# Performance work log

Measured on AMD Instinct MI355X. Metric: run time of the kernel, lower is better.

The kernel has to match this reference:

```python
import jax, jax.numpy as jnp
import numpy as np

N = 100000   # nodes
E = 800000   # undirected (unique) edges; directed count = 2*E
DV = 128; DE = 16; DH = 128; DO = 128
G = 64       # graphs in batch


def setup_inputs() -> dict:
    key = jax.random.key(0)
    ks = jax.random.split(key, 8)
    x = jax.random.normal(ks[0], (N, DV), jnp.float32)
    edge_index = jax.random.randint(ks[1], (2, 2 * E), 0, N, dtype=jnp.int32)
    edge_attr = jax.random.normal(ks[2], (E, DE), jnp.float32)
    batch = jnp.sort(jax.random.randint(ks[3], (N,), 0, G, dtype=jnp.int32))
    s = lambda k, shp, fan: jax.random.normal(k, shp, jnp.float32) / np.sqrt(fan)
    W_gcn = s(ks[4], (DV, DH), DV); b_gcn = jnp.zeros((DH,), jnp.float32)
    W_le = s(ks[5], (DE, DH), DE); b_le = jnp.zeros((DH,), jnp.float32)
    W_lin = s(ks[6], (2 * DH, DH), 2 * DH); b_lin = jnp.zeros((DH,), jnp.float32)
    W_out = s(ks[7], (DH, DO), DH); b_out = jnp.zeros((DO,), jnp.float32)
    return dict(x=x, edge_index=edge_index, edge_attr=edge_attr, batch=batch,
                W_gcn=W_gcn, b_gcn=b_gcn, W_le=W_le, b_le=b_le,
                W_lin=W_lin, b_lin=b_lin, W_out=W_out, b_out=b_out)


def reference(x, edge_index, edge_attr, batch,
              W_gcn, b_gcn, W_le, b_le, W_lin, b_lin, W_out, b_out):
    n = x.shape[0]
    loop = jnp.arange(n, dtype=edge_index.dtype)
    src = jnp.concatenate([edge_index[0], loop])  # [2E+N] with self loops
    dst = jnp.concatenate([edge_index[1], loop])

    # ---- GCNConv: symmetric norm, self-loops, lin then aggregate, + bias ----
    xw = x @ W_gcn                                      # [N, DH]
    ones_e = jnp.ones(src.shape[0], jnp.float32)
    deg = jax.ops.segment_sum(ones_e, dst, num_segments=n)  # >=1 via self loops
    dinv = jax.lax.rsqrt(deg)
    norm = dinv[src] * dinv[dst]                        # [2E+N]
    h = jax.ops.segment_sum(norm[:, None] * xw[src], dst, num_segments=n) + b_gcn
    h = jax.nn.relu(h)

    # ---- EdgeGCN: duplicate edge_attr per direction, self-loop attr = ones ----
    ea2 = jnp.repeat(edge_attr, 2, axis=0)              # [2E, DE] interleaved
    ea_full = jnp.concatenate([ea2, jnp.ones((n, edge_attr.shape[1]), jnp.float32)])
    edge_feat = ea_full @ W_le + b_le                   # [2E+N, DH]
    x_j = h[src]                                        # gather source node feats
    msg = jnp.concatenate([x_j, edge_feat], axis=-1) @ W_lin + b_lin
    h2 = jax.ops.segment_sum(msg, dst, num_segments=n)  # aggr='add'
    h2 = jax.nn.relu(h2)

    # ---- global mean pool + final linear ----
    cnt = jax.ops.segment_sum(jnp.ones(n, jnp.float32), batch, num_segments=G)
    pooled = jax.ops.segment_sum(h2, batch, num_segments=G) / jnp.maximum(cnt, 1.0)[:, None]
    return pooled @ W_out + b_out                       # [G, DO]
```

## Files before the change

### kernel.cpp

```cpp
#include <hip/hip_runtime.h>
#include <hip/hip_bf16.h>
#include <cstddef>

typedef unsigned int  u32;
typedef unsigned short u16;
typedef __attribute__((ext_vector_type(8))) short short8;
typedef __attribute__((ext_vector_type(4))) float f32x4;
typedef __attribute__((ext_vector_type(2))) float f32x2;

#define DV 128
#define DH 128
#define DE 16
#define DO 128
#define PSUB 32

__device__ inline float bf_lo(u32 u){ return __uint_as_float(u << 16); }
__device__ inline float bf_hi(u32 u){ return __uint_as_float(u & 0xFFFF0000u); }
__device__ inline u32 fpack2(float a, float b){
  u32 ua = __float_as_uint(a), ub = __float_as_uint(b);
  ua += 0x7FFFu + ((ua >> 16) & 1u);
  ub += 0x7FFFu + ((ub >> 16) & 1u);
  return (ua >> 16) | (ub & 0xFFFF0000u);
}
__device__ inline u16 f2bf(float a){
  u32 ua = __float_as_uint(a); ua += 0x7FFFu + ((ua >> 16) & 1u); return (u16)(ua >> 16);
}

__device__ inline void acc_fp8(u32 s, float& a0, float& a1, float& a2, float& a3){
  f32x2 lo = __builtin_amdgcn_cvt_pk_f32_fp8((int)s, false);
  f32x2 hi = __builtin_amdgcn_cvt_pk_f32_fp8((int)s, true);
  a0 += lo.x; a1 += lo.y; a2 += hi.x; a3 += hi.y;
}
__device__ inline u32 pack_fp8(float a0, float a1, float a2, float a3){
  int o = __builtin_amdgcn_cvt_pk_fp8_f32(a0, a1, 0, false);
  o = __builtin_amdgcn_cvt_pk_fp8_f32(a2, a3, o, true);
  return (u32)o;
}

__global__ void k_init(int* cnt, int n){
  int v = blockIdx.x * blockDim.x + threadIdx.x;
  if (v < n) cnt[v] = 0;
}
__global__ void k_count(const int* dst, int* cnt, int* rank, int e2){
  int j = blockIdx.x * blockDim.x + threadIdx.x;
  if (j < e2) rank[j] = atomicAdd(&cnt[dst[j]], 1);
}
__global__ __launch_bounds__(256) void k_scan1(const int* cnt, int* partial, int* bsums, int n){
  __shared__ int lds[256];
  int t = threadIdx.x;
  int base = blockIdx.x * 1024 + t * 4;
  int v0=0,v1=0,v2=0,v3=0;
  if (base + 3 < n){ int4 q = *(const int4*)(cnt + base); v0=q.x; v1=q.y; v2=q.z; v3=q.w; }
  else {
    if (base + 0 < n) v0 = cnt[base];
    if (base + 1 < n) v1 = cnt[base+1];
    if (base + 2 < n) v2 = cnt[base+2];
  }
  v0 = (v0 + 7) & ~7; v1 = (v1 + 7) & ~7; v2 = (v2 + 7) & ~7; v3 = (v3 + 7) & ~7;
  v1 += v0; v2 += v1; v3 += v2;
  lds[t] = v3; __syncthreads();
  for (int off = 1; off < 256; off <<= 1){
    int x = (t >= off) ? lds[t - off] : 0;
    __syncthreads();
    lds[t] += x;
    __syncthreads();
  }
  int add = (t > 0) ? lds[t - 1] : 0;
  if (base + 3 < n){
    int4 q; q.x = v0+add; q.y = v1+add; q.z = v2+add; q.w = v3+add;
    *(int4*)(partial + base) = q;
  } else {
    if (base + 0 < n) partial[base]   = v0 + add;
    if (base + 1 < n) partial[base+1] = v1 + add;
    if (base + 2 < n) partial[base+2] = v2 + add;
  }
  if (t == 255) bsums[blockIdx.x] = lds[255];
}
__global__ void k_scan2(const int* bsums, int* bexc, int nb){
  __shared__ int lds[128];
  int t = threadIdx.x;
  lds[t] = (t < nb) ? bsums[t] : 0;
  __syncthreads();
  for (int off = 1; off < 128; off <<= 1){
    int x = (t >= off) ? lds[t - off] : 0;
    __syncthreads();
    lds[t] += x;
    __syncthreads();
  }
  if (t < nb) bexc[t] = (t > 0) ? lds[t - 1] : 0;
}
__global__ void k_scan3(const int* partial, const int* bexc, int* row_ptr, int n){
  int i = blockIdx.x * blockDim.x + threadIdx.x;
  if (i < n) row_ptr[i + 1] = partial[i] + bexc[i >> 10];
  if (i == 0) row_ptr[0] = 0;
}
__global__ void k_prep(const int* cnt, float* dinv, float* degf, int n){
  int v = blockIdx.x * blockDim.x + threadIdx.x;
  if (v < n){
    float c = (float)(cnt[v] + 1);
    dinv[v] = rsqrtf(c);
    degf[v] = c;
  }
}
__global__ void k_scatter(const int* src, const int* dst, const int* rank,
                          const int* row_ptr, int2* ce, int e2){
  int j = blockIdx.x * blockDim.x + threadIdx.x;
  if (j < e2){
    int d = dst[j];
    int pos = row_ptr[d] + rank[j];
    ce[pos] = make_int2(src[j], j);
  }
}
__global__ void k_pad(const int* row_ptr, const int* cnt, int2* ce,
                      u32* xws_zrow, u32* h_zrow, int n){
  int v = blockIdx.x * blockDim.x + threadIdx.x;
  if (v < n){
    int s = row_ptr[v] + cnt[v], e = row_ptr[v + 1];
    for (int i = s; i < e; ++i) ce[i] = make_int2(n, 0);
  }
  if (blockIdx.x == 0 && threadIdx.x < 32){
    xws_zrow[threadIdx.x] = 0u;
    h_zrow[threadIdx.x] = 0u;
  }
}

__global__ __launch_bounds__(128) void k_wcombo(const float* W_lin, const float* b_lin,
                                                const float* W_le, const float* b_le, float* Wfull){
  int r = blockIdx.x, c = threadIdx.x;
  if (r < DH){
    Wfull[r * DH + c] = W_lin[r * DH + c];
  } else if (r < DH + DE){
    int i = r - DH;
    float acc = 0.f;
    #pragma unroll 8
    for (int k = 0; k < DH; k += 4){
      float4 wl = *(const float4*)(W_le + i * DH + k);
      acc += wl.x * W_lin[(size_t)(DH + k    ) * DH + c];
      acc += wl.y * W_lin[(size_t)(DH + k + 1) * DH + c];
      acc += wl.z * W_lin[(size_t)(DH + k + 2) * DH + c];
      acc += wl.w * W_lin[(size_t)(DH + k + 3) * DH + c];
    }
    Wfull[r * DH + c] = acc;
  } else if (r == 144){
    float acc = b_lin[c];
    #pragma unroll 8
    for (int k = 0; k < DH; k += 4){
      float4 bl = *(const float4*)(b_le + k);
      acc += bl.x * W_lin[(size_t)(DH + k    ) * DH + c];
      acc += bl.y * W_lin[(size_t)(DH + k + 1) * DH + c];
      acc += bl.z * W_lin[(size_t)(DH + k + 2) * DH + c];
      acc += bl.w * W_lin[(size_t)(DH + k + 3) * DH + c];
    }
    Wfull[r * DH + c] = acc;
  } else {
    Wfull[r * DH + c] = 0.f;
  }
}

template<int K, bool RELU, bool ABF16, bool SCALE, bool OFP8>
__global__ __launch_bounds__(256) void k_gemm_mfma(const void* Ap, const float* W, u32* outb,
                                                   const float* scale, int M){
  constexpr int SA = K + 8;
  constexpr int CS = 136;
  __shared__ u16 Wt[128 * SA];
  __shared__ u16 At[64 * SA];
  int tid = threadIdx.x;
  int row0 = blockIdx.x * 64;

  {
    int c = tid & 127, half = tid >> 7;
    for (int g = half; g < K / 8; g += 2){
      int k0 = g * 8;
      float w0 = W[(size_t)(k0+0)*128 + c], w1 = W[(size_t)(k0+1)*128 + c];
      float w2 = W[(size_t)(k0+2)*128 + c], w3 = W[(size_t)(k0+3)*128 + c];
      float w4 = W[(size_t)(k0+4)*128 + c], w5 = W[(size_t)(k0+5)*128 + c];
      float w6 = W[(size_t)(k0+6)*128 + c], w7 = W[(size_t)(k0+7)*128 + c];
      uint4 pk;
      pk.x = fpack2(w0, w1); pk.y = fpack2(w2, w3);
      pk.z = fpack2(w4, w5); pk.w = fpack2(w6, w7);
      *(uint4*)&Wt[c * SA + k0] = pk;
    }
  }
  constexpr int CH = K / 8;
  for (int idx = tid; idx < 64 * CH; idx += 256){
    int r = idx / CH, ch = idx - r * CH;
    int gr = row0 + r; if (gr > M - 1) gr = M - 1;
    uint4 pk;
    if (ABF16){
      pk = *(const uint4*)((const u16*)Ap + (size_t)gr * K + ch * 8);
    } else {
      const float* A = (const float*)Ap + (size_t)gr * K + ch * 8;
      float4 q0 = *(const float4*)A;
      float4 q1 = *(const float4*)(A + 4);
      pk.x = fpack2(q0.x, q0.y); pk.y = fpack2(q0.z, q0.w);
      pk.z = fpack2(q1.x, q1.y); pk.w = fpack2(q1.z, q1.w);
    }
    *(uint4*)&At[r * SA + ch * 8] = pk;
  }
  __syncthreads();

  int l = tid & 63, w = tid >> 6;
  int m = l & 15, quad = l >> 4;
  f32x4 acc[8];
  #pragma unroll
  for (int ct = 0; ct < 8; ++ct) acc[ct] = (f32x4){0.f, 0.f, 0.f, 0.f};
  #pragma unroll
  for (int ks = 0; ks < K; ks += 32){
    short8 av = *(const short8*)&At[(w * 16 + m) * SA + ks + quad * 8];
    #pragma unroll
    for (int ct = 0; ct < 8; ++ct){
      short8 bv = *(const short8*)&Wt[(ct * 16 + m) * SA + ks + quad * 8];
      acc[ct] = __builtin_amdgcn_mfma_f32_16x16x32_bf16(av, bv, acc[ct], 0, 0, 0);
    }
  }
  __syncthreads();

  u16* Ct = At;
  float sc[4];
  if (SCALE){
    #pragma unroll
    for (int r = 0; r < 4; ++r){
      int gr = row0 + w * 16 + quad * 4 + r;
      sc[r] = scale[gr < M ? gr : (M - 1)];
    }
  }
  #pragma unroll
  for (int ct = 0; ct < 8; ++ct){
    #pragma unroll
    for (int r = 0; r < 4; ++r){
      float vv = acc[ct][r];
      if (SCALE) vv *= sc[r];
      if (RELU)  vv = fmaxf(vv, 0.f);
      Ct[(w * 16 + quad * 4 + r) * CS + ct * 16 + m] = f2bf(vv);
    }
  }
  __syncthreads();
  if (OFP8){
    for (int idx = tid; idx < 64 * 16; idx += 256){
      int r = idx >> 4, c8 = idx & 15;
      int gr = row0 + r;
      if (gr < M){
        uint4 qv = *(const uint4*)&Ct[r * CS + c8 * 8];
        uint2 ov;
        ov.x = (u32)__builtin_amdgcn_cvt_pk_fp8_f32(bf_lo(qv.y), bf_hi(qv.y),
               __builtin_amdgcn_cvt_pk_fp8_f32(bf_lo(qv.x), bf_hi(qv.x), 0, false), true);
        ov.y = (u32)__builtin_amdgcn_cvt_pk_fp8_f32(bf_lo(qv.w), bf_hi(qv.w),
               __builtin_amdgcn_cvt_pk_fp8_f32(bf_lo(qv.z), bf_hi(qv.z), 0, false), true);
        *(uint2*)(outb + (size_t)gr * 32 + c8 * 2) = ov;
      }
    }
  } else {
    for (int idx = tid; idx < 64 * 16; idx += 256){
      int r = idx >> 4, ch = idx & 15;
      int gr = row0 + r;
      if (gr < M){
        uint4 q = *(const uint4*)&Ct[r * CS + ch * 8];
        *(uint4*)(outb + (size_t)gr * 64 + ch * 4) = q;
      }
    }
  }
}

__global__ __launch_bounds__(256) void k_phase1(const u32* xws8, const int* row_ptr, const int2* ce,
                                                const float* dinv, const float* b_gcn, u32* h8, int n){
  int lane = threadIdx.x & 63;
  int ln = lane & 31;
  int v = blockIdx.x * 8 + ((threadIdx.x >> 6) << 1) + (lane >> 5);
  if (v >= n) return;
  u32 sp = xws8[(size_t)v * 32 + ln];
  float a0 = 0.f, a1 = 0.f, a2 = 0.f, a3 = 0.f;
  acc_fp8(sp, a0, a1, a2, a3);
  int e0 = row_ptr[v], e1 = row_ptr[v + 1];
  int i = e0;
  u32 q0=0,q1=0,q2=0,q3=0,q4=0,q5=0,q6=0,q7=0;
  if (i < e1){
    const int4* cp = (const int4*)(ce + i);
    int4 A = cp[0], B = cp[1], C = cp[2], D = cp[3];
    q0 = xws8[(size_t)A.x * 32 + ln]; q1 = xws8[(size_t)A.z * 32 + ln];
    q2 = xws8[(size_t)B.x * 32 + ln]; q3 = xws8[(size_t)B.z * 32 + ln];
    q4 = xws8[(size_t)C.x * 32 + ln]; q5 = xws8[(size_t)C.z * 32 + ln];
    q6 = xws8[(size_t)D.x * 32 + ln]; q7 = xws8[(size_t)D.z * 32 + ln];
  }
  for (; i + 8 < e1; i += 8){
    const int4* cp2 = (const int4*)(ce + i + 8);
    int4 A = cp2[0], B = cp2[1], C = cp2[2], D = cp2[3];
    u32 p0 = xws8[(size_t)A.x * 32 + ln], p1 = xws8[(size_t)A.z * 32 + ln];
    u32 p2 = xws8[(size_t)B.x * 32 + ln], p3 = xws8[(size_t)B.z * 32 + ln];
    u32 p4 = xws8[(size_t)C.x * 32 + ln], p5 = xws8[(size_t)C.z * 32 + ln];
    u32 p6 = xws8[(size_t)D.x * 32 + ln], p7 = xws8[(size_t)D.z * 32 + ln];
    acc_fp8(q0, a0, a1, a2, a3); acc_fp8(q1, a0, a1, a2, a3);
    acc_fp8(q2, a0, a1, a2, a3); acc_fp8(q3, a0, a1, a2, a3);
    acc_fp8(q4, a0, a1, a2, a3); acc_fp8(q5, a0, a1, a2, a3);
    acc_fp8(q6, a0, a1, a2, a3); acc_fp8(q7, a0, a1, a2, a3);
    q0=p0; q1=p1; q2=p2; q3=p3; q4=p4; q5=p5; q6=p6; q7=p7;
  }
  if (i < e1){
    acc_fp8(q0, a0, a1, a2, a3); acc_fp8(q1, a0, a1, a2, a3);
    acc_fp8(q2, a0, a1, a2, a3); acc_fp8(q3, a0, a1, a2, a3);
    acc_fp8(q4, a0, a1, a2, a3); acc_fp8(q5, a0, a1, a2, a3);
    acc_fp8(q6, a0, a1, a2, a3); acc_fp8(q7, a0, a1, a2, a3);
  }
  float dv = dinv[v];
  float4 bg = *(const float4*)(b_gcn + ln * 4);
  a0 = fmaxf(fmaf(dv, a0, bg.x), 0.f);
  a1 = fmaxf(fmaf(dv, a1, bg.y), 0.f);
  a2 = fmaxf(fmaf(dv, a2, bg.z), 0.f);
  a3 = fmaxf(fmaf(dv, a3, bg.w), 0.f);
  h8[(size_t)v * 32 + ln] = pack_fp8(a0, a1, a2, a3);
}

__global__ __launch_bounds__(256) void k_phase2(const u32* h8, const int* row_ptr, const int2* ce,
                                                const float* edge_attr, const float* degf,
                                                u16* A2b, int n){
  int lane = threadIdx.x & 63;
  int ln = lane & 31;
  int half = lane >> 5;
  int v = blockIdx.x * 8 + ((threadIdx.x >> 6) << 1) + half;
  if (v >= n) return;
  u32 sp = h8[(size_t)v * 32 + ln];
  float a0 = 0.f, a1 = 0.f, a2 = 0.f, a3 = 0.f;
  acc_fp8(sp, a0, a1, a2, a3);
  float es = 0.f;
  int ch = ln & 15, grp = ln >> 4;
  int e0 = row_ptr[v], e1 = row_ptr[v + 1];
  int i = e0;
  u32 q0=0,q1=0,q2=0,q3=0,q4=0,q5=0,q6=0,q7=0;
  int4 A = {0,0,0,0}, B = {0,0,0,0}, C = {0,0,0,0}, D = {0,0,0,0};
  if (i < e1){
    const int4* cp = (const int4*)(ce + i);
    A = cp[0]; B = cp[1]; C = cp[2]; D = cp[3];
    q0 = h8[(size_t)A.x * 32 + ln]; q1 = h8[(size_t)A.z * 32 + ln];
    q2 = h8[(size_t)B.x * 32 + ln]; q3 = h8[(size_t)B.z * 32 + ln];
    q4 = h8[(size_t)C.x * 32 + ln]; q5 = h8[(size_t)C.z * 32 + ln];
    q6 = h8[(size_t)D.x * 32 + ln]; q7 = h8[(size_t)D.z * 32 + ln];
  }
  for (; i + 8 < e1; i += 8){
    const int4* cp2 = (const int4*)(ce + i + 8);
    int4 A2 = cp2[0], B2 = cp2[1], C2 = cp2[2], D2 = cp2[3];
    int s0x = grp ? C.x : A.x, s0y = grp ? C.y : A.y;
    int s1x = grp ? C.z : A.z, s1y = grp ? C.w : A.w;
    int s2x = grp ? D.x : B.x, s2y = grp ? D.y : B.y;
    int s3x = grp ? D.z : B.z, s3y = grp ? D.w : B.w;
    float v0 = edge_attr[(size_t)(s0y >> 1) * DE + ch];
    float v1 = edge_attr[(size_t)(s1y >> 1) * DE + ch];
    float v2 = edge_attr[(size_t)(s2y >> 1) * DE + ch];
    float v3 = edge_attr[(size_t)(s3y >> 1) * DE + ch];
    u32 p0 = h8[(size_t)A2.x * 32 + ln], p1 = h8[(size_t)A2.z * 32 + ln];
    u32 p2 = h8[(size_t)B2.x * 32 + ln], p3 = h8[(size_t)B2.z * 32 + ln];
    u32 p4 = h8[(size_t)C2.x * 32 + ln], p5 = h8[(size_t)C2.z * 32 + ln];
    u32 p6 = h8[(size_t)D2.x * 32 + ln], p7 = h8[(size_t)D2.z * 32 + ln];
    acc_fp8(q0, a0, a1, a2, a3); acc_fp8(q1, a0, a1, a2, a3);
    acc_fp8(q2, a0, a1, a2, a3); acc_fp8(q3, a0, a1, a2, a3);
    acc_fp8(q4, a0, a1, a2, a3); acc_fp8(q5, a0, a1, a2, a3);
    acc_fp8(q6, a0, a1, a2, a3); acc_fp8(q7, a0, a1, a2, a3);
    es = fmaf((s0x != n) ? 1.f : 0.f, v0, es);
    es = fmaf((s1x != n) ? 1.f : 0.f, v1, es);
    es = fmaf((s2x != n) ? 1.f : 0.f, v2, es);
    es = fmaf((s3x != n) ? 1.f : 0.f, v3, es);
    q0=p0; q1=p1; q2=p2; q3=p3; q4=p4; q5=p5; q6=p6; q7=p7;
    A=A2; B=B2; C=C2; D=D2;
  }
  if (i < e1){
    int s0x = grp ? C.x : A.x, s0y = grp ? C.y : A.y;
    int s1x = grp ? C.z : A.z, s1y = grp ? C.w : A.w;
    int s2x = grp ? D.x : B.x, s2y = grp ? D.y : B.y;
    int s3x = grp ? D.z : B.z, s3y = grp ? D.w : B.w;
    float v0 = edge_attr[(size_t)(s0y >> 1) * DE + ch];
    float v1 = edge_attr[(size_t)(s1y >> 1) * DE + ch];
    float v2 = edge_attr[(size_t)(s2y >> 1) * DE + ch];
    float v3 = edge_attr[(size_t)(s3y >> 1) * DE + ch];
    acc_fp8(q0, a0, a1, a2, a3); acc_fp8(q1, a0, a1, a2, a3);
    acc_fp8(q2, a0, a1, a2, a3); acc_fp8(q3, a0, a1, a2, a3);
    acc_fp8(q4, a0, a1, a2, a3); acc_fp8(q5, a0, a1, a2, a3);
    acc_fp8(q6, a0, a1, a2, a3); acc_fp8(q7, a0, a1, a2, a3);
    es = fmaf((s0x != n) ? 1.f : 0.f, v0, es);
    es = fmaf((s1x != n) ? 1.f : 0.f, v1, es);
    es = fmaf((s2x != n) ? 1.f : 0.f, v2, es);
    es = fmaf((s3x != n) ? 1.f : 0.f, v3, es);
  }
  es += __shfl_xor(es, 16);
  float c0v = __shfl(es, half * 32 + (ln & 7) * 2);
  float c1v = __shfl(es, half * 32 + (ln & 7) * 2 + 1);
  u32* rowp = (u32*)(A2b + (size_t)v * 160);
  uint2 o; o.x = fpack2(a0, a1); o.y = fpack2(a2, a3);
  *(uint2*)(rowp + ln * 2) = o;
  if (ln < 8){
    rowp[64 + ln] = fpack2(c0v + 1.0f, c1v + 1.0f);
  } else if (ln < 16){
    rowp[64 + ln] = (ln == 8) ? (u32)f2bf(degf[v]) : 0u;
  }
}

__global__ void k_starts(const int* batch, int* start, int n, int g){
  int v = blockIdx.x * blockDim.x + threadIdx.x;
  if (v >= n) return;
  int b = batch[v];
  int prev = (v == 0) ? -1 : batch[v - 1];
  for (int q = prev + 1; q <= b; ++q) start[q] = v;
  if (v == n - 1){ for (int q = b + 1; q <= g; ++q) start[q] = n; }
}
__global__ __launch_bounds__(256) void k_pool_a(const u32* h2_b, const int* start, float* partialp){
  __shared__ float2 red[256];
  int g = blockIdx.x >> 5;
  int s = blockIdx.x & (PSUB - 1);
  int s0 = start[g], s1 = start[g + 1];
  int tid = threadIdx.x;
  int cu = tid & 63, rr = tid >> 6;
  float ax = 0.f, ay = 0.f;
  for (int r = s0 + s * 4 + rr; r < s1; r += PSUB * 4){
    u32 q = h2_b[(size_t)r * 64 + cu];
    ax += bf_lo(q); ay += bf_hi(q);
  }
  red[tid] = make_float2(ax, ay);
  __syncthreads();
  if (rr == 0){
    #pragma unroll
    for (int p = 1; p < 4; p++){ float2 o = red[cu + (p << 6)]; ax += o.x; ay += o.y; }
    *(float2*)(partialp + (size_t)blockIdx.x * 128 + cu * 2) = make_float2(ax, ay);
  }
}
__global__ __launch_bounds__(128) void k_poolb_final(const float* partialp, const int* start,
                                                     const float* W_out, const float* b_out,
                                                     float* out){
  __shared__ float pl[DH];
  int g = blockIdx.x, c = threadIdx.x;
  float sum = 0.f;
  #pragma unroll 4
  for (int s = 0; s < PSUB; ++s) sum += partialp[((size_t)g * PSUB + s) * 128 + c];
  int cntg = start[g + 1] - start[g]; if (cntg < 1) cntg = 1;
  pl[c] = sum / (float)cntg;
  __syncthreads();
  float acc = b_out[c];
  for (int k = 0; k < DH; ++k) acc += pl[k] * W_out[k * DO + c];
  out[g * DO + c] = acc;
}

extern "C" void kernel_launch(void* const* d_in, const int* in_sizes, int n_in,
                              void* d_out, int out_size, void* d_ws, size_t ws_size,
                              hipStream_t stream){
  const float* x         = (const float*)d_in[0];
  const int*   edge_index= (const int*)  d_in[1];
  const float* edge_attr = (const float*)d_in[2];
  const int*   batch     = (const int*)  d_in[3];
  const float* W_gcn     = (const float*)d_in[4];
  const float* b_gcn     = (const float*)d_in[5];
  const float* W_le      = (const float*)d_in[6];
  const float* b_le      = (const float*)d_in[7];
  const float* W_lin     = (const float*)d_in[8];
  const float* b_lin     = (const float*)d_in[9];
  const float* W_out     = (const float*)d_in[10];
  const float* b_out     = (const float*)d_in[11];
  float* out = (float*)d_out;

  const int n  = in_sizes[0] / DV;
  const int e2 = in_sizes[1] / 2;
  const int g  = out_size / DO;
  const int* srcp = edge_index;
  const int* dstp = edge_index + e2;
  const int e2pad = e2 + 7 * n + 8;

  char* ws = (char*)d_ws;
  size_t off = 0;
  auto alloc = [&](size_t bytes) -> char* {
    char* p = ws + off; off = (off + bytes + 255) & ~(size_t)255; return p;
  };

  int*   cnt     = (int*)  alloc((size_t)n * 4);
  int*   row_ptr = (int*)  alloc((size_t)(n + 1) * 4);
  int*   rank    = (int*)  alloc((size_t)e2 * 4);
  int*   partial = (int*)  alloc((size_t)n * 4);
  int*   bsums   = (int*)  alloc(512);
  int*   bexc    = (int*)  alloc(512);
  float* dinv    = (float*)alloc((size_t)n * 4);
  float* degf    = (float*)alloc((size_t)n * 4);
  int*   startg  = (int*)  alloc((size_t)(g + 1) * 4);
  float* partialp= (float*)alloc((size_t)g * PSUB * 128 * 4);
  float* Wfull   = (float*)alloc(160 * DH * 4);
  u32*   h8      = (u32*)  alloc((size_t)(n + 1) * 128);
  int2*  ce      = (int2*) alloc((size_t)e2pad * 8);
  u32*   h2_b    = (u32*)  alloc((size_t)n * 64 * 4);
  size_t szXW = (size_t)(n + 1) * 128, szA2 = (size_t)n * 160 * 2;
  char* regionA = alloc(szA2 > szXW ? szA2 : szXW);
  u32* xws8 = (u32*)regionA;
  u16* A2b  = (u16*)regionA;

  const int nb1024 = (n + 1023) / 1024;

  k_init   <<<(n + 255) / 256, 256, 0, stream>>>(cnt, n);
  k_count  <<<(e2 + 255) / 256, 256, 0, stream>>>(dstp, cnt, rank, e2);
  k_scan1  <<<nb1024, 256, 0, stream>>>(cnt, partial, bsums, n);
  k_scan2  <<<1, 128, 0, stream>>>(bsums, bexc, nb1024);
  k_scan3  <<<(n + 255) / 256, 256, 0, stream>>>(partial, bexc, row_ptr, n);
  k_prep   <<<(n + 255) / 256, 256, 0, stream>>>(cnt, dinv, degf, n);
  k_scatter<<<(e2 + 255) / 256, 256, 0, stream>>>(srcp, dstp, rank, row_ptr, ce, e2);
  k_pad    <<<(n + 255) / 256, 256, 0, stream>>>(row_ptr, cnt, ce,
                                                 xws8 + (size_t)n * 32, h8 + (size_t)n * 32, n);
  k_wcombo <<<160, 128, 0, stream>>>(W_lin, b_lin, W_le, b_le, Wfull);

  k_gemm_mfma<DV, false, false, true, true><<<(n + 63) / 64, 256, 0, stream>>>(x, W_gcn, xws8, dinv, n);
  k_phase1 <<<(n + 7) / 8, 256, 0, stream>>>(xws8, row_ptr, ce, dinv, b_gcn, h8, n);
  k_phase2 <<<(n + 7) / 8, 256, 0, stream>>>(h8, row_ptr, ce, edge_attr, degf, A2b, n);
  k_gemm_mfma<160, true, true, false, false><<<(n + 63) / 64, 256, 0, stream>>>(A2b, Wfull, h2_b, (const float*)nullptr, n);

  k_starts      <<<(n + 255) / 256, 256, 0, stream>>>(batch, startg, n, g);
  k_pool_a      <<<g * PSUB, 256, 0, stream>>>(h2_b, startg, partialp);
  k_poolb_final <<<g, 128, 0, stream>>>(partialp, startg, W_out, b_out, out);
}
```

Measured before the change: 414.8 us.

## Fuse phase2 aggregation with the second GEMM via LDS staging

Phase2 aggregation now writes each 64-node tile's aggregated features and edge sums into shared memory, and the same block runs the 160-wide MFMA GEMM with ReLU directly. This removes the bf16 A2b intermediate round trip through global memory and one kernel launch. k_prep is also folded into k_scan3, and the accumulators use packed f32x2 adds. In exchange, each block stages the weights in two K chunks with extra barriers. The larger LDS footprint and the gather phase being serialized before the GEMM inside each block may reduce occupancy and latency hiding.

```diff
diff --git a/kernel.cpp b/kernel.cpp
--- a/kernel.cpp
+++ b/kernel.cpp
@@ -26,10 +26,9 @@
   u32 ua = __float_as_uint(a); ua += 0x7FFFu + ((ua >> 16) & 1u); return (u16)(ua >> 16);
 }
 
-__device__ inline void acc_fp8(u32 s, float& a0, float& a1, float& a2, float& a3){
-  f32x2 lo = __builtin_amdgcn_cvt_pk_f32_fp8((int)s, false);
-  f32x2 hi = __builtin_amdgcn_cvt_pk_f32_fp8((int)s, true);
-  a0 += lo.x; a1 += lo.y; a2 += hi.x; a3 += hi.y;
+__device__ inline void acc_fp8v(u32 s, f32x2& lo, f32x2& hi){
+  lo += __builtin_amdgcn_cvt_pk_f32_fp8((int)s, false);
+  hi += __builtin_amdgcn_cvt_pk_f32_fp8((int)s, true);
 }
 __device__ inline u32 pack_fp8(float a0, float a1, float a2, float a3){
   int o = __builtin_amdgcn_cvt_pk_fp8_f32(a0, a1, 0, false);
@@ -89,18 +88,16 @@
   }
   if (t < nb) bexc[t] = (t > 0) ? lds[t - 1] : 0;
 }
-__global__ void k_scan3(const int* partial, const int* bexc, int* row_ptr, int n){
+__global__ void k_scan3(const int* partial, const int* bexc, const int* cnt,
+                        int* row_ptr, float* dinv, float* degf, int n){
   int i = blockIdx.x * blockDim.x + threadIdx.x;
-  if (i < n) row_ptr[i + 1] = partial[i] + bexc[i >> 10];
+  if (i < n){
+    row_ptr[i + 1] = partial[i] + bexc[i >> 10];
+    float c = (float)(cnt[i] + 1);
+    dinv[i] = rsqrtf(c);
+    degf[i] = c;
+  }
   if (i == 0) row_ptr[0] = 0;
-}
-__global__ void k_prep(const int* cnt, float* dinv, float* degf, int n){
-  int v = blockIdx.x * blockDim.x + threadIdx.x;
-  if (v < n){
-    float c = (float)(cnt[v] + 1);
-    dinv[v] = rsqrtf(c);
-    degf[v] = c;
-  }
 }
 __global__ void k_scatter(const int* src, const int* dst, const int* rank,
                           const int* row_ptr, int2* ce, int e2){
@@ -166,7 +163,6 @@
   __shared__ u16 At[64 * SA];
   int tid = threadIdx.x;
   int row0 = blockIdx.x * 64;
-
   {
     int c = tid & 127, half = tid >> 7;
     for (int g = half; g < K / 8; g += 2){
@@ -198,7 +194,6 @@
     *(uint4*)&At[r * SA + ch * 8] = pk;
   }
   __syncthreads();
-
   int l = tid & 63, w = tid >> 6;
   int m = l & 15, quad = l >> 4;
   f32x4 acc[8];
@@ -214,7 +209,6 @@
     }
   }
   __syncthreads();
-
   u16* Ct = At;
   float sc[4];
   if (SCALE){
@@ -267,9 +261,8 @@
   int ln = lane & 31;
   int v = blockIdx.x * 8 + ((threadIdx.x >> 6) << 1) + (lane >> 5);
   if (v >= n) return;
-  u32 sp = xws8[(size_t)v * 32 + ln];
-  float a0 = 0.f, a1 = 0.f, a2 = 0.f, a3 = 0.f;
-  acc_fp8(sp, a0, a1, a2, a3);
+  f32x2 alo = {0.f, 0.f}, ahi = {0.f, 0.f};
+  acc_fp8v(xws8[(size_t)v * 32 + ln], alo, ahi);
   int e0 = row_ptr[v], e1 = row_ptr[v + 1];
   int i = e0;
   u32 q0=0,q1=0,q2=0,q3=0,q4=0,q5=0,q6=0,q7=0;
@@ -288,106 +281,173 @@
     u32 p2 = xws8[(size_t)B.x * 32 + ln], p3 = xws8[(size_t)B.z * 32 + ln];
     u32 p4 = xws8[(size_t)C.x * 32 + ln], p5 = xws8[(size_t)C.z * 32 + ln];
     u32 p6 = xws8[(size_t)D.x * 32 + ln], p7 = xws8[(size_t)D.z * 32 + ln];
-    acc_fp8(q0, a0, a1, a2, a3); acc_fp8(q1, a0, a1, a2, a3);
-    acc_fp8(q2, a0, a1, a2, a3); acc_fp8(q3, a0, a1, a2, a3);
-    acc_fp8(q4, a0, a1, a2, a3); acc_fp8(q5, a0, a1, a2, a3);
-    acc_fp8(q6, a0, a1, a2, a3); acc_fp8(q7, a0, a1, a2, a3);
+    acc_fp8v(q0, alo, ahi); acc_fp8v(q1, alo, ahi);
+    acc_fp8v(q2, alo, ahi); acc_fp8v(q3, alo, ahi);
+    acc_fp8v(q4, alo, ahi); acc_fp8v(q5, alo, ahi);
+    acc_fp8v(q6, alo, ahi); acc_fp8v(q7, alo, ahi);
     q0=p0; q1=p1; q2=p2; q3=p3; q4=p4; q5=p5; q6=p6; q7=p7;
   }
   if (i < e1){
-    acc_fp8(q0, a0, a1, a2, a3); acc_fp8(q1, a0, a1, a2, a3);
-    acc_fp8(q2, a0, a1, a2, a3); acc_fp8(q3, a0, a1, a2, a3);
-    acc_fp8(q4, a0, a1, a2, a3); acc_fp8(q5, a0, a1, a2, a3);
-    acc_fp8(q6, a0, a1, a2, a3); acc_fp8(q7, a0, a1, a2, a3);
+    acc_fp8v(q0, alo, ahi); acc_fp8v(q1, alo, ahi);
+    acc_fp8v(q2, alo, ahi); acc_fp8v(q3, alo, ahi);
+    acc_fp8v(q4, alo, ahi); acc_fp8v(q5, alo, ahi);
+    acc_fp8v(q6, alo, ahi); acc_fp8v(q7, alo, ahi);
   }
   float dv = dinv[v];
   float4 bg = *(const float4*)(b_gcn + ln * 4);
-  a0 = fmaxf(fmaf(dv, a0, bg.x), 0.f);
-  a1 = fmaxf(fmaf(dv, a1, bg.y), 0.f);
-  a2 = fmaxf(fmaf(dv, a2, bg.z), 0.f);
-  a3 = fmaxf(fmaf(dv, a3, bg.w), 0.f);
+  float a0 = fmaxf(fmaf(dv, alo.x, bg.x), 0.f);
+  float a1 = fmaxf(fmaf(dv, alo.y, bg.y), 0.f);
+  float a2 = fmaxf(fmaf(dv, ahi.x, bg.z), 0.f);
+  float a3 = fmaxf(fmaf(dv, ahi.y, bg.w), 0.f);
   h8[(size_t)v * 32 + ln] = pack_fp8(a0, a1, a2, a3);
 }
 
-__global__ __launch_bounds__(256) void k_phase2(const u32* h8, const int* row_ptr, const int2* ce,
-                                                const float* edge_attr, const float* degf,
-                                                u16* A2b, int n){
-  int lane = threadIdx.x & 63;
-  int ln = lane & 31;
-  int half = lane >> 5;
-  int v = blockIdx.x * 8 + ((threadIdx.x >> 6) << 1) + half;
-  if (v >= n) return;
-  u32 sp = h8[(size_t)v * 32 + ln];
-  float a0 = 0.f, a1 = 0.f, a2 = 0.f, a3 = 0.f;
-  acc_fp8(sp, a0, a1, a2, a3);
-  float es = 0.f;
+__global__ __launch_bounds__(256) void k_phase2g(const u32* h8, const int* row_ptr, const int2* ce,
+                                                 const float* edge_attr, const float* degf,
+                                                 const float* Wfull, u32* h2b, int n){
+  constexpr int SA = 168;
+  constexpr int SW = 104;
+  constexpr int CS = 136;
+  __shared__ u16 At[64 * SA];
+  __shared__ u16 Wt[128 * SW];
+  int tid = threadIdx.x;
+  int w = tid >> 6;
+  int lane = tid & 63;
+  int ln = lane & 31, half = lane >> 5;
+  int row0 = blockIdx.x * 64;
   int ch = ln & 15, grp = ln >> 4;
-  int e0 = row_ptr[v], e1 = row_ptr[v + 1];
-  int i = e0;
-  u32 q0=0,q1=0,q2=0,q3=0,q4=0,q5=0,q6=0,q7=0;
-  int4 A = {0,0,0,0}, B = {0,0,0,0}, C = {0,0,0,0}, D = {0,0,0,0};
-  if (i < e1){
-    const int4* cp = (const int4*)(ce + i);
-    A = cp[0]; B = cp[1]; C = cp[2]; D = cp[3];
-    q0 = h8[(size_t)A.x * 32 + ln]; q1 = h8[(size_t)A.z * 32 + ln];
-    q2 = h8[(size_t)B.x * 32 + ln]; q3 = h8[(size_t)B.z * 32 + ln];
-    q4 = h8[(size_t)C.x * 32 + ln]; q5 = h8[(size_t)C.z * 32 + ln];
-    q6 = h8[(size_t)D.x * 32 + ln]; q7 = h8[(size_t)D.z * 32 + ln];
-  }
-  for (; i + 8 < e1; i += 8){
-    const int4* cp2 = (const int4*)(ce + i + 8);
-    int4 A2 = cp2[0], B2 = cp2[1], C2 = cp2[2], D2 = cp2[3];
-    int s0x = grp ? C.x : A.x, s0y = grp ? C.y : A.y;
-    int s1x = grp ? C.z : A.z, s1y = grp ? C.w : A.w;
-    int s2x = grp ? D.x : B.x, s2y = grp ? D.y : B.y;
-    int s3x = grp ? D.z : B.z, s3y = grp ? D.w : B.w;
-    float v0 = edge_attr[(size_t)(s0y >> 1) * DE + ch];
-    float v1 = edge_attr[(size_t)(s1y >> 1) * DE + ch];
-    float v2 = edge_attr[(size_t)(s2y >> 1) * DE + ch];
-    float v3 = edge_attr[(size_t)(s3y >> 1) * DE + ch];
-    u32 p0 = h8[(size_t)A2.x * 32 + ln], p1 = h8[(size_t)A2.z * 32 + ln];
-    u32 p2 = h8[(size_t)B2.x * 32 + ln], p3 = h8[(size_t)B2.z * 32 + ln];
-    u32 p4 = h8[(size_t)C2.x * 32 + ln], p5 = h8[(size_t)C2.z * 32 + ln];
-    u32 p6 = h8[(size_t)D2.x * 32 + ln], p7 = h8[(size_t)D2.z * 32 + ln];
-    acc_fp8(q0, a0, a1, a2, a3); acc_fp8(q1, a0, a1, a2, a3);
-    acc_fp8(q2, a0, a1, a2, a3); acc_fp8(q3, a0, a1, a2, a3);
-    acc_fp8(q4, a0, a1, a2, a3); acc_fp8(q5, a0, a1, a2, a3);
-    acc_fp8(q6, a0, a1, a2, a3); acc_fp8(q7, a0, a1, a2, a3);
-    es = fmaf((s0x != n) ? 1.f : 0.f, v0, es);
-    es = fmaf((s1x != n) ? 1.f : 0.f, v1, es);
-    es = fmaf((s2x != n) ? 1.f : 0.f, v2, es);
-    es = fmaf((s3x != n) ? 1.f : 0.f, v3, es);
-    q0=p0; q1=p1; q2=p2; q3=p3; q4=p4; q5=p5; q6=p6; q7=p7;
-    A=A2; B=B2; C=C2; D=D2;
-  }
-  if (i < e1){
-    int s0x = grp ? C.x : A.x, s0y = grp ? C.y : A.y;
-    int s1x = grp ? C.z : A.z, s1y = grp ? C.w : A.w;
-    int s2x = grp ? D.x : B.x, s2y = grp ? D.y : B.y;
-    int s3x = grp ? D.z : B.z, s3y = grp ? D.w : B.w;
-    float v0 = edge_attr[(size_t)(s0y >> 1) * DE + ch];
-    float v1 = edge_attr[(size_t)(s1y >> 1) * DE + ch];
-    float v2 = edge_attr[(size_t)(s2y >> 1) * DE + ch];
-    float v3 = edge_attr[(size_t)(s3y >> 1) * DE + ch];
-    acc_fp8(q0, a0, a1, a2, a3); acc_fp8(q1, a0, a1, a2, a3);
-    acc_fp8(q2, a0, a1, a2, a3); acc_fp8(q3, a0, a1, a2, a3);
-    acc_fp8(q4, a0, a1, a2, a3); acc_fp8(q5, a0, a1, a2, a3);
-    acc_fp8(q6, a0, a1, a2, a3); acc_fp8(q7, a0, a1, a2, a3);
-    es = fmaf((s0x != n) ? 1.f : 0.f, v0, es);
-    es = fmaf((s1x != n) ? 1.f : 0.f, v1, es);
-    es = fmaf((s2x != n) ? 1.f : 0.f, v2, es);
-    es = fmaf((s3x != n) ? 1.f : 0.f, v3, es);
-  }
-  es += __shfl_xor(es, 16);
-  float c0v = __shfl(es, half * 32 + (ln & 7) * 2);
-  float c1v = __shfl(es, half * 32 + (ln & 7) * 2 + 1);
-  u32* rowp = (u32*)(A2b + (size_t)v * 160);
-  uint2 o; o.x = fpack2(a0, a1); o.y = fpack2(a2, a3);
-  *(uint2*)(rowp + ln * 2) = o;
-  if (ln < 8){
-    rowp[64 + ln] = fpack2(c0v + 1.0f, c1v + 1.0f);
-  } else if (ln < 16){
-    rowp[64 + ln] = (ln == 8) ? (u32)f2bf(degf[v]) : 0u;
+
+  for (int pair = 0; pair < 8; ++pair){
+    int lr = w * 16 + pair * 2 + half;
+    int v = row0 + lr;
+    u32* rowp = (u32*)&At[lr * SA];
+    if (v >= n){
+      for (int ii = ln; ii < 80; ii += 32) rowp[ii] = 0u;
+      continue;
+    }
+    f32x2 alo = {0.f, 0.f}, ahi = {0.f, 0.f};
+    acc_fp8v(h8[(size_t)v * 32 + ln], alo, ahi);
+    float es = 0.f;
+    int e0 = row_ptr[v], e1 = row_ptr[v + 1];
+    int i = e0;
+    u32 q0=0,q1=0,q2=0,q3=0,q4=0,q5=0,q6=0,q7=0;
+    int4 A = {0,0,0,0}, B = {0,0,0,0}, C = {0,0,0,0}, D = {0,0,0,0};
+    if (i < e1){
+      const int4* cp = (const int4*)(ce + i);
+      A = cp[0]; B = cp[1]; C = cp[2]; D = cp[3];
+      q0 = h8[(size_t)A.x * 32 + ln]; q1 = h8[(size_t)A.z * 32 + ln];
+      q2 = h8[(size_t)B.x * 32 + ln]; q3 = h8[(size_t)B.z * 32 + ln];
+      q4 = h8[(size_t)C.x * 32 + ln]; q5 = h8[(size_t)C.z * 32 + ln];
+      q6 = h8[(size_t)D.x * 32 + ln]; q7 = h8[(size_t)D.z * 32 + ln];
+    }
+    for (; i + 8 < e1; i += 8){
+      const int4* cp2 = (const int4*)(ce + i + 8);
+      int4 A2 = cp2[0], B2 = cp2[1], C2 = cp2[2], D2 = cp2[3];
+      int s0x = grp ? C.x : A.x, s0y = grp ? C.y : A.y;
+      int s1x = grp ? C.z : A.z, s1y = grp ? C.w : A.w;
+      int s2x = grp ? D.x : B.x, s2y = grp ? D.y : B.y;
+      int s3x = grp ? D.z : B.z, s3y = grp ? D.w : B.w;
+      float v0 = edge_attr[(size_t)(s0y >> 1) * DE + ch];
+      float v1 = edge_attr[(size_t)(s1y >> 1) * DE + ch];
+      float v2 = edge_attr[(size_t)(s2y >> 1) * DE + ch];
+      float v3 = edge_attr[(size_t)(s3y >> 1) * DE + ch];
+      u32 p0 = h8[(size_t)A2.x * 32 + ln], p1 = h8[(size_t)A2.z * 32 + ln];
+      u32 p2 = h8[(size_t)B2.x * 32 + ln], p3 = h8[(size_t)B2.z * 32 + ln];
+      u32 p4 = h8[(size_t)C2.x * 32 + ln], p5 = h8[(size_t)C2.z * 32 + ln];
+      u32 p6 = h8[(size_t)D2.x * 32 + ln], p7 = h8[(size_t)D2.z * 32 + ln];
+      acc_fp8v(q0, alo, ahi); acc_fp8v(q1, alo, ahi);
+      acc_fp8v(q2, alo, ahi); acc_fp8v(q3, alo, ahi);
+      acc_fp8v(q4, alo, ahi); acc_fp8v(q5, alo, ahi);
+      acc_fp8v(q6, alo, ahi); acc_fp8v(q7, alo, ahi);
+      es = fmaf((s0x != n) ? 1.f : 0.f, v0, es);
+      es = fmaf((s1x != n) ? 1.f : 0.f, v1, es);
+      es = fmaf((s2x != n) ? 1.f : 0.f, v2, es);
+      es = fmaf((s3x != n) ? 1.f : 0.f, v3, es);
+      q0=p0; q1=p1; q2=p2; q3=p3; q4=p4; q5=p5; q6=p6; q7=p7;
+      A=A2; B=B2; C=C2; D=D2;
+    }
+    if (i < e1){
+      int s0x = grp ? C.x : A.x, s0y = grp ? C.y : A.y;
+      int s1x = grp ? C.z : A.z, s1y = grp ? C.w : A.w;
+      int s2x = grp ? D.x : B.x, s2y = grp ? D.y : B.y;
+      int s3x = grp ? D.z : B.z, s3y = grp ? D.w : B.w;
+      float v0 = edge_attr[(size_t)(s0y >> 1) * DE + ch];
+      float v1 = edge_attr[(size_t)(s1y >> 1) * DE + ch];
+      float v2 = edge_attr[(size_t)(s2y >> 1) * DE + ch];
+      float v3 = edge_attr[(size_t)(s3y >> 1) * DE + ch];
+      acc_fp8v(q0, alo, ahi); acc_fp8v(q1, alo, ahi);
+      acc_fp8v(q2, alo, ahi); acc_fp8v(q3, alo, ahi);
+      acc_fp8v(q4, alo, ahi); acc_fp8v(q5, alo, ahi);
+      acc_fp8v(q6, alo, ahi); acc_fp8v(q7, alo, ahi);
+      es = fmaf((s0x != n) ? 1.f : 0.f, v0, es);
+      es = fmaf((s1x != n) ? 1.f : 0.f, v1, es);
+      es = fmaf((s2x != n) ? 1.f : 0.f, v2, es);
+      es = fmaf((s3x != n) ? 1.f : 0.f, v3, es);
+    }
+    es += __shfl_xor(es, 16);
+    float c0v = __shfl(es, half * 32 + (ln & 7) * 2);
+    float c1v = __shfl(es, half * 32 + (ln & 7) * 2 + 1);
+    uint2 o; o.x = fpack2(alo.x, alo.y); o.y = fpack2(ahi.x, ahi.y);
+    *(uint2*)(rowp + ln * 2) = o;
+    if (ln < 8){
+      rowp[64 + ln] = fpack2(c0v + 1.0f, c1v + 1.0f);
+    } else if (ln < 16){
+      rowp[64 + ln] = (ln == 8) ? (u32)f2bf(degf[v]) : 0u;
+    }
+  }
+
+  int m = lane & 15, quad = lane >> 4;
+  f32x4 acc[8];
+  #pragma unroll
+  for (int ct = 0; ct < 8; ++ct) acc[ct] = (f32x4){0.f, 0.f, 0.f, 0.f};
+  #pragma unroll
+  for (int c = 0; c < 2; ++c){
+    int kbase = c ? 96 : 0;
+    int klen  = c ? 64 : 96;
+    __syncthreads();
+    {
+      int col = tid & 127, hf = tid >> 7;
+      for (int g = hf; g < klen / 8; g += 2){
+        int k0 = kbase + g * 8;
+        float w0 = Wfull[(size_t)(k0+0)*128 + col], w1 = Wfull[(size_t)(k0+1)*128 + col];
+        float w2 = Wfull[(size_t)(k0+2)*128 + col], w3 = Wfull[(size_t)(k0+3)*128 + col];
+        float w4 = Wfull[(size_t)(k0+4)*128 + col], w5 = Wfull[(size_t)(k0+5)*128 + col];
+        float w6 = Wfull[(size_t)(k0+6)*128 + col], w7 = Wfull[(size_t)(k0+7)*128 + col];
+        uint4 pk;
+        pk.x = fpack2(w0, w1); pk.y = fpack2(w2, w3);
+        pk.z = fpack2(w4, w5); pk.w = fpack2(w6, w7);
+        *(uint4*)&Wt[col * SW + g * 8] = pk;
+      }
+    }
+    __syncthreads();
+    for (int ks = 0; ks < klen; ks += 32){
+      short8 av = *(const short8*)&At[(w * 16 + m) * SA + kbase + ks + quad * 8];
+      #pragma unroll
+      for (int ct = 0; ct < 8; ++ct){
+        short8 bv = *(const short8*)&Wt[(ct * 16 + m) * SW + ks + quad * 8];
+        acc[ct] = __builtin_amdgcn_mfma_f32_16x16x32_bf16(av, bv, acc[ct], 0, 0, 0);
+      }
+    }
+  }
+  __syncthreads();
+
+  u16* Ct = Wt;
+  #pragma unroll
+  for (int ct = 0; ct < 8; ++ct){
+    #pragma unroll
+    for (int r = 0; r < 4; ++r){
+      float vv = fmaxf(acc[ct][r], 0.f);
+      Ct[(w * 16 + quad * 4 + r) * CS + ct * 16 + m] = f2bf(vv);
+    }
+  }
+  __syncthreads();
+  for (int idx = tid; idx < 64 * 16; idx += 256){
+    int r = idx >> 4, c8 = idx & 15;
+    int gr = row0 + r;
+    if (gr < n){
+      uint4 q = *(const uint4*)&Ct[r * CS + c8 * 8];
+      *(uint4*)(h2b + (size_t)gr * 64 + c8 * 4) = q;
+    }
   }
 }
 
@@ -477,12 +537,9 @@
   float* partialp= (float*)alloc((size_t)g * PSUB * 128 * 4);
   float* Wfull   = (float*)alloc(160 * DH * 4);
   u32*   h8      = (u32*)  alloc((size_t)(n + 1) * 128);
+  u32*   xws8    = (u32*)  alloc((size_t)(n + 1) * 128);
   int2*  ce      = (int2*) alloc((size_t)e2pad * 8);
   u32*   h2_b    = (u32*)  alloc((size_t)n * 64 * 4);
-  size_t szXW = (size_t)(n + 1) * 128, szA2 = (size_t)n * 160 * 2;
-  char* regionA = alloc(szA2 > szXW ? szA2 : szXW);
-  u32* xws8 = (u32*)regionA;
-  u16* A2b  = (u16*)regionA;
 
   const int nb1024 = (n + 1023) / 1024;
 
@@ -490,8 +547,7 @@
   k_count  <<<(e2 + 255) / 256, 256, 0, stream>>>(dstp, cnt, rank, e2);
   k_scan1  <<<nb1024, 256, 0, stream>>>(cnt, partial, bsums, n);
   k_scan2  <<<1, 128, 0, stream>>>(bsums, bexc, nb1024);
-  k_scan3  <<<(n + 255) / 256, 256, 0, stream>>>(partial, bexc, row_ptr, n);
-  k_prep   <<<(n + 255) / 256, 256, 0, stream>>>(cnt, dinv, degf, n);
+  k_scan3  <<<(n + 255) / 256, 256, 0, stream>>>(partial, bexc, cnt, row_ptr, dinv, degf, n);
   k_scatter<<<(e2 + 255) / 256, 256, 0, stream>>>(srcp, dstp, rank, row_ptr, ce, e2);
   k_pad    <<<(n + 255) / 256, 256, 0, stream>>>(row_ptr, cnt, ce,
                                                  xws8 + (size_t)n * 32, h8 + (size_t)n * 32, n);
@@ -499,8 +555,7 @@
 
   k_gemm_mfma<DV, false, false, true, true><<<(n + 63) / 64, 256, 0, stream>>>(x, W_gcn, xws8, dinv, n);
   k_phase1 <<<(n + 7) / 8, 256, 0, stream>>>(xws8, row_ptr, ce, dinv, b_gcn, h8, n);
-  k_phase2 <<<(n + 7) / 8, 256, 0, stream>>>(h8, row_ptr, ce, edge_attr, degf, A2b, n);
-  k_gemm_mfma<160, true, true, false, false><<<(n + 63) / 64, 256, 0, stream>>>(A2b, Wfull, h2_b, (const float*)nullptr, n);
+  k_phase2g<<<(n + 63) / 64, 256, 0, stream>>>(h8, row_ptr, ce, edge_attr, degf, Wfull, h2_b, n);
 
   k_starts      <<<(n + 255) / 256, 256, 0, stream>>>(batch, startg, n, g);
   k_pool_a      <<<g * PSUB, 256, 0, stream>>>(h2_b, startg, partialp);
```

Result: slower. 428.7 us (+3.4%).
